# Kernel optimization log

Hardware: AMD Instinct MI355X
Metric: run time of the kernel (lower is better)

Reference implementation:

```python
import jax, jax.numpy as jnp
import numpy as np

T, B, D_IN, D_HID, D_OUT = 512, 64, 512, 512, 512


def setup_inputs() -> dict:
    key = jax.random.key(0)
    k_x, k_xh, k_hh, k_o = jax.random.split(key, 4)
    return {
        "x": jax.random.normal(k_x, (T, B, D_IN), dtype=jnp.float32),
        "xh": jax.random.normal(k_xh, (D_IN, D_HID), dtype=jnp.float32) * 0.01,
        "hh": jax.random.normal(k_hh, (D_HID, D_HID), dtype=jnp.float32) * 0.01,
        "hb": jnp.zeros((D_HID,), dtype=jnp.float32),
        "o": jax.random.normal(k_o, (D_HID, D_OUT), dtype=jnp.float32) * 0.01,
        "h0": jnp.zeros((1, D_HID), dtype=jnp.float32),
    }


def reference(x, xh, hh, hb, o, h0):
    # Elman RNN (training branch): h_t = relu(x_t @ xh + h_{t-1} @ hh + hb); y_t = h_t @ o
    # h starts as (1, hid) and broadcasts to (B, hid) at step 1, as in the torch code.
    batch = x.shape[1]
    h_init = jnp.broadcast_to(h0, (batch, h0.shape[1]))

    def step(h, xi):  # xi: [B, D_IN], h: [B, D_HID]
        h = jax.nn.relu(xi @ xh + h @ hh + hb)
        return h, h @ o  # y: [B, D_OUT]

    _, ys = jax.lax.scan(step, h_init, x)
    return ys  # [T, B, D_OUT] (stacked version of the torch list of outputs)
```

## Files before the change

kernel.cpp:

```cpp
#include <hip/hip_runtime.h>
#include <hip/hip_bf16.h>

#define TSTEPS 512
#define BATCH  64
#define DIM    512
#define NWG    8

using short8 = __attribute__((ext_vector_type(8))) short;
using f32x4  = __attribute__((ext_vector_type(4))) float;

__device__ __forceinline__ unsigned short f2bf(float f) {
    unsigned u = __builtin_bit_cast(unsigned, f);
    unsigned r = (u + 0x7FFFu + ((u >> 16) & 1u)) >> 16;
    return (unsigned short)r;
}

__global__ void conv_T(const float* __restrict__ src, unsigned short* __restrict__ dst) {
    __shared__ float tile[32][33];
    const int bx = blockIdx.x * 32, by = blockIdx.y * 32;
    const int tx = threadIdx.x & 31, ty = threadIdx.x >> 5;
#pragma unroll
    for (int k = 0; k < 32; k += 8)
        tile[ty + k][tx] = src[(size_t)(by + ty + k) * DIM + bx + tx];
    __syncthreads();
#pragma unroll
    for (int k = 0; k < 32; k += 8)
        dst[(size_t)(bx + ty + k) * DIM + by + tx] = f2bf(tile[tx][ty + k]);
}

__global__ __launch_bounds__(256) void gemm_xwm(
    const float* __restrict__ X,
    const unsigned short* __restrict__ Bt,
    const float* __restrict__ bias, float* __restrict__ Out)
{
    __shared__ unsigned short As[128 * 40];
    __shared__ unsigned short Bs[128 * 40];
    const int tid = threadIdx.x;
    const int m0 = blockIdx.x * 128, n0 = blockIdx.y * 128;
    const int lane = tid & 63, wv = tid >> 6;
    const int ln15 = lane & 15, kg = lane >> 4;
    const int wr = (wv >> 1) * 64, wc = (wv & 1) * 64;

    f32x4 acc[4][4];
#pragma unroll
    for (int m = 0; m < 4; ++m)
#pragma unroll
        for (int n = 0; n < 4; ++n) acc[m][n] = f32x4{0.f, 0.f, 0.f, 0.f};

    const int arow = tid >> 1, ahalf = tid & 1;
    for (int k0 = 0; k0 < DIM; k0 += 32) {
        const float4* ga = reinterpret_cast<const float4*>(
            X + (size_t)(m0 + arow) * DIM + k0 + ahalf * 16);
        float4 a0 = ga[0], a1 = ga[1], a2 = ga[2], a3 = ga[3];
        const ulonglong2* gb = reinterpret_cast<const ulonglong2*>(
            Bt + (size_t)(n0 + arow) * DIM + k0 + ahalf * 16);
        ulonglong2 bv0 = gb[0], bv1 = gb[1];
        __syncthreads();
        {
            unsigned long long p[4];
            const float4 av[4] = {a0, a1, a2, a3};
#pragma unroll
            for (int q = 0; q < 4; ++q)
                p[q] = (unsigned long long)f2bf(av[q].x)
                     | ((unsigned long long)f2bf(av[q].y) << 16)
                     | ((unsigned long long)f2bf(av[q].z) << 32)
                     | ((unsigned long long)f2bf(av[q].w) << 48);
            unsigned long long* s = reinterpret_cast<unsigned long long*>(&As[arow * 40 + ahalf * 16]);
            s[0] = p[0]; s[1] = p[1]; s[2] = p[2]; s[3] = p[3];
            *reinterpret_cast<ulonglong2*>(&Bs[arow * 40 + ahalf * 16]) = bv0;
            *reinterpret_cast<ulonglong2*>(&Bs[arow * 40 + ahalf * 16 + 8]) = bv1;
        }
        __syncthreads();
        short8 af[4], bf[4];
#pragma unroll
        for (int m = 0; m < 4; ++m)
            af[m] = *reinterpret_cast<const short8*>(&As[(wr + m * 16 + ln15) * 40 + kg * 8]);
#pragma unroll
        for (int n = 0; n < 4; ++n)
            bf[n] = *reinterpret_cast<const short8*>(&Bs[(wc + n * 16 + ln15) * 40 + kg * 8]);
#pragma unroll
        for (int m = 0; m < 4; ++m)
#pragma unroll
            for (int n = 0; n < 4; ++n)
                acc[m][n] = __builtin_amdgcn_mfma_f32_16x16x32_bf16(af[m], bf[n], acc[m][n], 0, 0, 0);
    }
    float4* Out4 = reinterpret_cast<float4*>(Out);
#pragma unroll
    for (int n = 0; n < 4; ++n) {
        int col = n0 + wc + n * 16 + ln15;
        float bb = bias[col];
#pragma unroll
        for (int m = 0; m < 4; ++m) {
            int t = (m0 + wr) >> 6;
            float4 v;
            v.x = acc[m][n][0] + bb; v.y = acc[m][n][1] + bb;
            v.z = acc[m][n][2] + bb; v.w = acc[m][n][3] + bb;
            Out4[(((size_t)t * 4 + kg) * 4 + m) * DIM + col] = v;
        }
    }
}

__global__ __launch_bounds__(256, 1) void rnn_scan(
    const float* __restrict__ hh, const float* __restrict__ xwb,
    const float* __restrict__ h0, unsigned long long* __restrict__ histU,
    unsigned int* __restrict__ flags)
{
    const int tid  = threadIdx.x;
    const int wg   = blockIdx.x;
    const int lane = tid & 63;
    const int wv   = __builtin_amdgcn_readfirstlane(tid >> 6);
    const int ln15 = lane & 15, kg = lane >> 4;
    const int colw = wg * 64 + wv * 16 + ln15;

    __shared__ unsigned long long hsU[BATCH * DIM / 4];

    short8 Bhh[16];
#pragma unroll
    for (int kk = 0; kk < 16; ++kk) {
        short8 bh;
#pragma unroll
        for (int j = 0; j < 8; ++j) {
            int k = kk * 32 + kg * 8 + j;
            bh[j] = (short)f2bf(hh[(size_t)k * DIM + colw]);
        }
        Bhh[kk] = bh;
    }

    {
        unsigned long long* dst = histU + wv * 2048 + lane;
#pragma unroll 4
        for (int i = 0; i < 32; ++i) {
            float4 f = *reinterpret_cast<const float4*>(h0 + ((i & 1) << 8) + lane * 4);
            unsigned long long v = (unsigned long long)f2bf(f.x)
                | ((unsigned long long)f2bf(f.y) << 16)
                | ((unsigned long long)f2bf(f.z) << 32)
                | ((unsigned long long)f2bf(f.w) << 48);
            __hip_atomic_store(dst + i * 64, v, __ATOMIC_RELAXED, __HIP_MEMORY_SCOPE_AGENT);
        }
    }
    asm volatile("s_waitcnt vmcnt(0)" ::: "memory");
    __syncthreads();

    const float4* xw4 = reinterpret_cast<const float4*>(xwb);
    f32x4 xwr[4];
#pragma unroll
    for (int m = 0; m < 4; ++m) {
        float4 v = xw4[(((size_t)0 * 4 + kg) * 4 + m) * DIM + colw];
        xwr[m] = f32x4{v.x, v.y, v.z, v.w};
    }

    for (int t = 0; t < TSTEPS; ++t) {
        {
            const unsigned long long* src = histU + (size_t)t * 8192 + wv * 2048 + lane;
#pragma unroll
            for (int ii = 0; ii < 32; ii += 8) {
                unsigned long long v[8];
#pragma unroll
                for (int j = 0; j < 8; ++j)
                    v[j] = __hip_atomic_load(src + (ii + j) * 64, __ATOMIC_RELAXED, __HIP_MEMORY_SCOPE_AGENT);
#pragma unroll
                for (int j = 0; j < 8; ++j) {
                    int i = ii + j;
                    int row = (wv << 4) + (i >> 1);
                    int byte = ((row << 10) + ((i & 1) << 9) + (lane << 3)) ^ ((row & 7) << 4);
                    hsU[byte >> 3] = v[j];
                }
            }
        }
        __syncthreads();

        f32x4 acch[4];
#pragma unroll
        for (int m = 0; m < 4; ++m) acch[m] = f32x4{0.f, 0.f, 0.f, 0.f};
#pragma unroll
        for (int kk = 0; kk < 16; ++kk) {
#pragma unroll
            for (int m = 0; m < 4; ++m) {
                int row = m * 16 + ln15;
                int byte = ((row << 10) + (kk << 6) + (kg << 4)) ^ ((row & 7) << 4);
                short8 a = *reinterpret_cast<const short8*>(
                    reinterpret_cast<const char*>(hsU) + byte);
                acch[m] = __builtin_amdgcn_mfma_f32_16x16x32_bf16(a, Bhh[kk], acch[m], 0, 0, 0);
            }
        }

        {
            unsigned short* hdst = reinterpret_cast<unsigned short*>(histU + (size_t)(t + 1) * 8192);
#pragma unroll
            for (int m = 0; m < 4; ++m)
#pragma unroll
                for (int r = 0; r < 4; ++r) {
                    int row = m * 16 + kg * 4 + r;
                    float hn = xwr[m][r] + acch[m][r];
                    hn = hn > 0.f ? hn : 0.f;
                    __hip_atomic_store(hdst + (size_t)row * DIM + colw, f2bf(hn),
                                       __ATOMIC_RELAXED, __HIP_MEMORY_SCOPE_AGENT);
                }
        }
        asm volatile("s_waitcnt vmcnt(0)" ::: "memory");
        __syncthreads();
        if (tid == 0)
            __hip_atomic_store(&flags[wg], (unsigned)(t + 1),
                               __ATOMIC_RELAXED, __HIP_MEMORY_SCOPE_AGENT);

        if (t < TSTEPS - 1) {
#pragma unroll
            for (int m = 0; m < 4; ++m) {
                float4 v = xw4[(((size_t)(t + 1) * 4 + kg) * 4 + m) * DIM + colw];
                xwr[m] = f32x4{v.x, v.y, v.z, v.w};
            }
            if (wv == 0) {
                for (;;) {
                    unsigned f = __hip_atomic_load(&flags[lane & (NWG - 1)],
                                                   __ATOMIC_RELAXED, __HIP_MEMORY_SCOPE_AGENT);
                    if (!__any(f < (unsigned)(t + 1))) break;
                    __builtin_amdgcn_s_sleep(1);
                }
            }
            __syncthreads();
        }
    }
}

__global__ __launch_bounds__(256) void gemm_y(
    const unsigned short* __restrict__ A,
    const unsigned short* __restrict__ Bt,
    float* __restrict__ Out)
{
    __shared__ unsigned short As[128 * 40];
    __shared__ unsigned short Bs[128 * 40];
    const int tid = threadIdx.x;
    const int m0 = blockIdx.x * 128, n0 = blockIdx.y * 128;
    const int lane = tid & 63, wv = tid >> 6;
    const int ln15 = lane & 15, kg = lane >> 4;
    const int wr = (wv >> 1) * 64, wc = (wv & 1) * 64;

    f32x4 acc[4][4];
#pragma unroll
    for (int m = 0; m < 4; ++m)
#pragma unroll
        for (int n = 0; n < 4; ++n) acc[m][n] = f32x4{0.f, 0.f, 0.f, 0.f};

    const int sr = tid & 127;
    for (int k0 = 0; k0 < DIM; k0 += 32) {
        const unsigned short* g = (tid < 128)
            ? A  + (size_t)(m0 + sr) * DIM + k0
            : Bt + (size_t)(n0 + sr) * DIM + k0;
        unsigned short* s = (tid < 128) ? &As[sr * 40] : &Bs[sr * 40];
        ulonglong2 v0 = reinterpret_cast<const ulonglong2*>(g)[0];
        ulonglong2 v1 = reinterpret_cast<const ulonglong2*>(g)[1];
        ulonglong2 v2 = reinterpret_cast<const ulonglong2*>(g)[2];
        ulonglong2 v3 = reinterpret_cast<const ulonglong2*>(g)[3];
        __syncthreads();
        reinterpret_cast<ulonglong2*>(s)[0] = v0;
        reinterpret_cast<ulonglong2*>(s)[1] = v1;
        reinterpret_cast<ulonglong2*>(s)[2] = v2;
        reinterpret_cast<ulonglong2*>(s)[3] = v3;
        __syncthreads();
        short8 af[4], bf[4];
#pragma unroll
        for (int m = 0; m < 4; ++m)
            af[m] = *reinterpret_cast<const short8*>(&As[(wr + m * 16 + ln15) * 40 + kg * 8]);
#pragma unroll
        for (int n = 0; n < 4; ++n)
            bf[n] = *reinterpret_cast<const short8*>(&Bs[(wc + n * 16 + ln15) * 40 + kg * 8]);
#pragma unroll
        for (int m = 0; m < 4; ++m)
#pragma unroll
            for (int n = 0; n < 4; ++n)
                acc[m][n] = __builtin_amdgcn_mfma_f32_16x16x32_bf16(af[m], bf[n], acc[m][n], 0, 0, 0);
    }
#pragma unroll
    for (int m = 0; m < 4; ++m)
#pragma unroll
        for (int n = 0; n < 4; ++n)
#pragma unroll
            for (int r = 0; r < 4; ++r) {
                int row = m0 + wr + m * 16 + kg * 4 + r;
                int col = n0 + wc + n * 16 + ln15;
                Out[(size_t)row * DIM + col] = acc[m][n][r];
            }
}

extern "C" void kernel_launch(void* const* d_in, const int* in_sizes, int n_in,
                              void* d_out, int out_size, void* d_ws, size_t ws_size,
                              hipStream_t stream) {
    const float* x  = (const float*)d_in[0];
    const float* xh = (const float*)d_in[1];
    const float* hh = (const float*)d_in[2];
    const float* hb = (const float*)d_in[3];
    const float* o  = (const float*)d_in[4];
    const float* h0 = (const float*)d_in[5];
    float* out = (float*)d_out;

    unsigned int* flags = (unsigned int*)d_ws;
    unsigned long long* histU = (unsigned long long*)((char*)d_ws + 4096);
    unsigned short* oT  = (unsigned short*)((char*)d_ws + 4096 + (size_t)513 * 65536);
    unsigned short* xhT = oT + (size_t)DIM * DIM;

    (void)hipMemsetAsync(d_ws, 0, 256, stream);
    conv_T<<<dim3(16, 16), 256, 0, stream>>>(o, oT);
    conv_T<<<dim3(16, 16), 256, 0, stream>>>(xh, xhT);
    gemm_xwm<<<dim3(256, 4), 256, 0, stream>>>(x, xhT, hb, out);
    rnn_scan<<<NWG, 256, 0, stream>>>(hh, out, h0, histU, flags);
    gemm_y<<<dim3(256, 4), 256, 0, stream>>>(
        (const unsigned short*)histU + 32768, oT, out);
}
```

Baseline: 2.154 ms.

## Replace per-step flag barrier with tagged data words in a triple-buffered exchange

The separate flag array and its global barrier are removed from the recurrent scan. Each step's hidden state is now published as 64-bit words that pack two bf16 values with a step tag, in a three-slot ring buffer. Consumers poll the data words until every tag matches, which drops the store-drain wait, the flag write and the extra __syncthreads round trips per step. LDS is double-buffered so the next step's copy-in does not overwrite data still being read. The cost is more bytes per exchanged value (the tag), a separate plain write of history for the output GEMM, and a correctness dependence on relaxed-ordering tag visibility.

```diff
diff --git a/kernel.cpp b/kernel.cpp
--- a/kernel.cpp
+++ b/kernel.cpp
@@ -102,8 +102,8 @@
 
 __global__ __launch_bounds__(256, 1) void rnn_scan(
     const float* __restrict__ hh, const float* __restrict__ xwb,
-    const float* __restrict__ h0, unsigned long long* __restrict__ histU,
-    unsigned int* __restrict__ flags)
+    const float* __restrict__ h0, unsigned long long* __restrict__ tbuf,
+    unsigned short* __restrict__ hist)
 {
     const int tid  = threadIdx.x;
     const int wg   = blockIdx.x;
@@ -112,7 +112,7 @@
     const int ln15 = lane & 15, kg = lane >> 4;
     const int colw = wg * 64 + wv * 16 + ln15;
 
-    __shared__ unsigned long long hsU[BATCH * DIM / 4];
+    __shared__ unsigned long long hsU[2 * 8192];
 
     short8 Bhh[16];
 #pragma unroll
@@ -127,44 +127,50 @@
     }
 
     {
-        unsigned long long* dst = histU + wv * 2048 + lane;
-#pragma unroll 4
-        for (int i = 0; i < 32; ++i) {
-            float4 f = *reinterpret_cast<const float4*>(h0 + ((i & 1) << 8) + lane * 4);
-            unsigned long long v = (unsigned long long)f2bf(f.x)
-                | ((unsigned long long)f2bf(f.y) << 16)
-                | ((unsigned long long)f2bf(f.z) << 32)
-                | ((unsigned long long)f2bf(f.w) << 48);
-            __hip_atomic_store(dst + i * 64, v, __ATOMIC_RELAXED, __HIP_MEMORY_SCOPE_AGENT);
-        }
-    }
-    asm volatile("s_waitcnt vmcnt(0)" ::: "memory");
-    __syncthreads();
+        int colp = wg * 32 + (tid & 31);
+        unsigned pair = (unsigned)f2bf(h0[2 * colp]) | ((unsigned)f2bf(h0[2 * colp + 1]) << 16);
+        unsigned long long v = (unsigned long long)pair | (1ull << 32);
+#pragma unroll
+        for (int q = 0; q < 8; ++q) {
+            int row = (tid >> 5) * 8 + q;
+            __hip_atomic_store(&tbuf[row * 256 + colp], v,
+                               __ATOMIC_RELAXED, __HIP_MEMORY_SCOPE_AGENT);
+        }
+    }
 
     const float4* xw4 = reinterpret_cast<const float4*>(xwb);
-    f32x4 xwr[4];
-#pragma unroll
-    for (int m = 0; m < 4; ++m) {
-        float4 v = xw4[(((size_t)0 * 4 + kg) * 4 + m) * DIM + colw];
-        xwr[m] = f32x4{v.x, v.y, v.z, v.w};
-    }
 
     for (int t = 0; t < TSTEPS; ++t) {
-        {
-            const unsigned long long* src = histU + (size_t)t * 8192 + wv * 2048 + lane;
-#pragma unroll
-            for (int ii = 0; ii < 32; ii += 8) {
-                unsigned long long v[8];
-#pragma unroll
-                for (int j = 0; j < 8; ++j)
-                    v[j] = __hip_atomic_load(src + (ii + j) * 64, __ATOMIC_RELAXED, __HIP_MEMORY_SCOPE_AGENT);
-#pragma unroll
-                for (int j = 0; j < 8; ++j) {
-                    int i = ii + j;
-                    int row = (wv << 4) + (i >> 1);
-                    int byte = ((row << 10) + ((i & 1) << 9) + (lane << 3)) ^ ((row & 7) << 4);
-                    hsU[byte >> 3] = v[j];
-                }
+        f32x4 xwr[4];
+#pragma unroll
+        for (int m = 0; m < 4; ++m) {
+            float4 v = xw4[(((size_t)t * 4 + kg) * 4 + m) * DIM + colw];
+            xwr[m] = f32x4{v.x, v.y, v.z, v.w};
+        }
+
+        const unsigned long long* src = tbuf + (size_t)(t % 3) * 16384 + tid;
+        const unsigned expect = (unsigned)(t + 1);
+        char* lbase = reinterpret_cast<char*>(hsU) + (t & 1) * 65536;
+#pragma unroll 1
+        for (int half = 0; half < 2; ++half) {
+            unsigned long long va[32];
+            for (;;) {
+#pragma unroll
+                for (int a = 0; a < 32; ++a)
+                    va[a] = __hip_atomic_load(src + (half * 32 + a) * 256,
+                                              __ATOMIC_RELAXED, __HIP_MEMORY_SCOPE_AGENT);
+                unsigned acc = 0;
+#pragma unroll
+                for (int a = 0; a < 32; ++a)
+                    acc |= ((unsigned)(va[a] >> 32)) ^ expect;
+                if (!__any((acc & 0xffffu) != 0)) break;
+                __builtin_amdgcn_s_sleep(1);
+            }
+#pragma unroll
+            for (int a = 0; a < 32; ++a) {
+                int row = half * 32 + a;
+                int byte = ((row << 10) + (tid << 2)) ^ ((row & 7) << 4);
+                *reinterpret_cast<unsigned*>(lbase + byte) = (unsigned)va[a];
             }
         }
         __syncthreads();
@@ -178,47 +184,32 @@
             for (int m = 0; m < 4; ++m) {
                 int row = m * 16 + ln15;
                 int byte = ((row << 10) + (kk << 6) + (kg << 4)) ^ ((row & 7) << 4);
-                short8 a = *reinterpret_cast<const short8*>(
-                    reinterpret_cast<const char*>(hsU) + byte);
+                short8 a = *reinterpret_cast<const short8*>(lbase + byte);
                 acch[m] = __builtin_amdgcn_mfma_f32_16x16x32_bf16(a, Bhh[kk], acch[m], 0, 0, 0);
             }
         }
 
-        {
-            unsigned short* hdst = reinterpret_cast<unsigned short*>(histU + (size_t)(t + 1) * 8192);
-#pragma unroll
-            for (int m = 0; m < 4; ++m)
-#pragma unroll
-                for (int r = 0; r < 4; ++r) {
-                    int row = m * 16 + kg * 4 + r;
-                    float hn = xwr[m][r] + acch[m][r];
-                    hn = hn > 0.f ? hn : 0.f;
-                    __hip_atomic_store(hdst + (size_t)row * DIM + colw, f2bf(hn),
+        const unsigned long long tagbits = ((unsigned long long)(t + 2)) << 32;
+        unsigned long long* tdst = tbuf + (size_t)((t + 1) % 3) * 16384;
+        unsigned short* hdst = hist + (size_t)(t + 1) * (BATCH * DIM);
+        const bool evenlane = (ln15 & 1) == 0;
+        const int colp = colw >> 1;
+#pragma unroll
+        for (int m = 0; m < 4; ++m)
+#pragma unroll
+            for (int r = 0; r < 4; ++r) {
+                int row = m * 16 + kg * 4 + r;
+                float hn = xwr[m][r] + acch[m][r];
+                hn = hn > 0.f ? hn : 0.f;
+                unsigned self = f2bf(hn);
+                hdst[(size_t)row * DIM + colw] = (unsigned short)self;
+                unsigned partner = (unsigned)__shfl_xor((int)self, 1);
+                unsigned pair = evenlane ? (self | (partner << 16))
+                                         : (partner | (self << 16));
+                if (evenlane == (m < 2))
+                    __hip_atomic_store(&tdst[row * 256 + colp], tagbits | (unsigned long long)pair,
                                        __ATOMIC_RELAXED, __HIP_MEMORY_SCOPE_AGENT);
-                }
-        }
-        asm volatile("s_waitcnt vmcnt(0)" ::: "memory");
-        __syncthreads();
-        if (tid == 0)
-            __hip_atomic_store(&flags[wg], (unsigned)(t + 1),
-                               __ATOMIC_RELAXED, __HIP_MEMORY_SCOPE_AGENT);
-
-        if (t < TSTEPS - 1) {
-#pragma unroll
-            for (int m = 0; m < 4; ++m) {
-                float4 v = xw4[(((size_t)(t + 1) * 4 + kg) * 4 + m) * DIM + colw];
-                xwr[m] = f32x4{v.x, v.y, v.z, v.w};
-            }
-            if (wv == 0) {
-                for (;;) {
-                    unsigned f = __hip_atomic_load(&flags[lane & (NWG - 1)],
-                                                   __ATOMIC_RELAXED, __HIP_MEMORY_SCOPE_AGENT);
-                    if (!__any(f < (unsigned)(t + 1))) break;
-                    __builtin_amdgcn_s_sleep(1);
-                }
-            }
-            __syncthreads();
-        }
+            }
     }
 }
 
@@ -293,16 +284,15 @@
     const float* h0 = (const float*)d_in[5];
     float* out = (float*)d_out;
 
-    unsigned int* flags = (unsigned int*)d_ws;
-    unsigned long long* histU = (unsigned long long*)((char*)d_ws + 4096);
-    unsigned short* oT  = (unsigned short*)((char*)d_ws + 4096 + (size_t)513 * 65536);
+    unsigned long long* tbuf = (unsigned long long*)d_ws;
+    unsigned short* hist = (unsigned short*)((char*)d_ws + 393216);
+    unsigned short* oT  = (unsigned short*)((char*)d_ws + 393216 + (size_t)513 * 65536);
     unsigned short* xhT = oT + (size_t)DIM * DIM;
 
-    (void)hipMemsetAsync(d_ws, 0, 256, stream);
+    (void)hipMemsetAsync(d_ws, 0, 393216, stream);
     conv_T<<<dim3(16, 16), 256, 0, stream>>>(o, oT);
     conv_T<<<dim3(16, 16), 256, 0, stream>>>(xh, xhT);
     gemm_xwm<<<dim3(256, 4), 256, 0, stream>>>(x, xhT, hb, out);
-    rnn_scan<<<NWG, 256, 0, stream>>>(hh, out, h0, histU, flags);
-    gemm_y<<<dim3(256, 4), 256, 0, stream>>>(
-        (const unsigned short*)histU + 32768, oT, out);
-}
+    rnn_scan<<<NWG, 256, 0, stream>>>(hh, out, h0, tbuf, hist);
+    gemm_y<<<dim3(256, 4), 256, 0, stream>>>(hist + 32768, oT, out);
+}
```

Measured after the change: 2.487 ms. 1.15x slower.
